# Optimization experiments

Hardware: AMD Instinct MI355X
Metric: run time of the kernel (lower is better)

Reference implementation:

```python
import jax, jax.numpy as jnp
import numpy as np

N_CODES = 1024
CODE_DIM = 256

def setup_inputs() -> dict:
    key = jax.random.key(0)
    k1, k2 = jax.random.split(key)
    z_e = jax.random.normal(k1, (16, 1024, CODE_DIM), dtype=jnp.float32)
    codebook = jax.random.normal(k2, (N_CODES, CODE_DIM), dtype=jnp.float32)
    return {"z_e": z_e, "codebook": codebook}

def reference(z_e, codebook):
    # ||z - c||^2 = ||z||^2 - 2 z.c + ||c||^2 ; ||z||^2 is constant over codes,
    # so argmin only needs -2 z.c + ||c||^2. Avoids the [B,N,n_codes,D] broadcast.
    dots = jnp.einsum('bnd,kd->bnk', z_e, codebook)          # [B, N, n_codes]
    c_sq = jnp.sum(codebook * codebook, axis=-1)             # [n_codes]
    scores = c_sq[None, None, :] - 2.0 * dots
    indices = jnp.argmin(scores, axis=-1)                    # [B, N] int
    z_q = codebook[indices]                                  # gather [B, N, D]
    # straight-through estimator
    z_q = z_e + jax.lax.stop_gradient(z_q - z_e)
    return (z_q, indices)
```

## Files before the change

### kernel.cpp

```cpp
#include <hip/hip_runtime.h>


#define M_ROWS 16384
#define DDIM   256
#define NCODES 1024

typedef _Float16 half8 __attribute__((ext_vector_type(8)));
typedef float    f32x4 __attribute__((ext_vector_type(4)));

__device__ __forceinline__ unsigned umin2(unsigned a, unsigned b) { return a < b ? a : b; }
__device__ __forceinline__ unsigned umax2(unsigned a, unsigned b) { return a > b ? a : b; }
__device__ __forceinline__ void top2_merge(unsigned& k0, unsigned& k1,
                                           unsigned o0, unsigned o1) {
    const unsigned t = umax2(k0, o0);
    k0 = umin2(k0, o0);
    k1 = umin2(t, umin2(k1, o1));
}

#define DPP_SELF(k, ctrl) \
    ((unsigned)__builtin_amdgcn_update_dpp((int)(k), (int)(k), (ctrl), 0xF, 0xF, false))
#define DPP_Z(v, ctrl) \
    __builtin_amdgcn_update_dpp(0, (v), (ctrl), 0xF, 0xF, true)

__device__ __forceinline__ float dpp_radd(float x) {
    float s = x;
    s += __int_as_float(DPP_Z(__float_as_int(s), 0x111));
    s += __int_as_float(DPP_Z(__float_as_int(s), 0x112));
    s += __int_as_float(DPP_Z(__float_as_int(s), 0x114));
    s += __int_as_float(DPP_Z(__float_as_int(s), 0x118));
    s += __int_as_float(DPP_Z(__float_as_int(s), 0x142));
    s += __int_as_float(DPP_Z(__float_as_int(s), 0x143));
    return s;
}

__global__ __launch_bounds__(256) void vq_prep_cb(const float* __restrict__ cb,
                                                  _Float16* __restrict__ chp,
                                                  float* __restrict__ csq) {
    if (blockIdx.x < 128) {
        const int gid = blockIdx.x * 256 + threadIdx.x;
        const int l   = gid & 63;
        const int g   = gid >> 6;
        const int kt  = g & 7;
        const int rt  = g >> 3;
        const int row = rt * 16 + (l & 15);
        const int k0  = kt * 32 + (l >> 4) * 8;
        const float4 v0 = *reinterpret_cast<const float4*>(cb + (size_t)row * DDIM + k0);
        const float4 v1 = *reinterpret_cast<const float4*>(cb + (size_t)row * DDIM + k0 + 4);
        half8 h;
        h[0] = (_Float16)v0.x; h[1] = (_Float16)v0.y; h[2] = (_Float16)v0.z; h[3] = (_Float16)v0.w;
        h[4] = (_Float16)v1.x; h[5] = (_Float16)v1.y; h[6] = (_Float16)v1.z; h[7] = (_Float16)v1.w;
        *reinterpret_cast<half8*>(chp + (size_t)gid * 8) = h;
    } else {
        const int code = (blockIdx.x - 128) * 4 + (threadIdx.x >> 6);
        const int lane = threadIdx.x & 63;
        const float4 v = *reinterpret_cast<const float4*>(cb + (size_t)code * DDIM + lane * 4);
        float s = v.x * v.x + v.y * v.y + v.z * v.z + v.w * v.w;
        s = dpp_radd(s);
        if (lane == 63) csq[code] = s;
    }
}

__global__ __launch_bounds__(1024) void vq_fused(const float* __restrict__ z,
                                                 const _Float16* __restrict__ Bp,
                                                 const float* __restrict__ cb,
                                                 const float* __restrict__ csq,
                                                 float* __restrict__ zq,
                                                 float* __restrict__ outIdx) {
    __shared__ __align__(16) _Float16 Ah[64 * 256];
    __shared__ uint2 red[16][64];

    const int tid  = threadIdx.x;
    const int lane = tid & 63;
    const int wv   = tid >> 6;
    const int rowBase = blockIdx.x * 64;

#pragma unroll
    for (int i = 0; i < 2; ++i) {
        const int slot = i * 1024 + tid;
        const int l  = slot & 63;
        const int g  = slot >> 6;
        const int m  = g >> 3;
        const int kt = g & 7;
        const int row = rowBase + m * 16 + (l & 15);
        const int k0  = kt * 32 + (l >> 4) * 8;
        const float4 v0 = *reinterpret_cast<const float4*>(z + (size_t)row * DDIM + k0);
        const float4 v1 = *reinterpret_cast<const float4*>(z + (size_t)row * DDIM + k0 + 4);
        half8 h;
        h[0] = (_Float16)(-v0.x); h[1] = (_Float16)(-v0.y);
        h[2] = (_Float16)(-v0.z); h[3] = (_Float16)(-v0.w);
        h[4] = (_Float16)(-v1.x); h[5] = (_Float16)(-v1.y);
        h[6] = (_Float16)(-v1.z); h[7] = (_Float16)(-v1.w);
        *reinterpret_cast<half8*>(&Ah[g * 512 + l * 8]) = h;
    }
    __syncthreads();

    const half8* __restrict__ B = reinterpret_cast<const half8*>(Bp);
    const int cx = lane & 15;
    const int q  = lane >> 4;
    const int colTile = wv;
    const int colBase = colTile * 64;

    unsigned idxv[4];
    float    bias[4];
#pragma unroll
    for (int n = 0; n < 4; ++n) {
        idxv[n] = (unsigned)(colBase + n * 16 + cx);
        bias[n] = 0.5f * csq[idxv[n]];
    }

    f32x4 acc[4][4];
#pragma unroll
    for (int m = 0; m < 4; ++m)
#pragma unroll
        for (int n = 0; n < 4; ++n)
            acc[m][n] = (f32x4){bias[n], bias[n], bias[n], bias[n]};

#pragma unroll
    for (int kt = 0; kt < 8; ++kt) {
        half8 a[4], b[4];
#pragma unroll
        for (int m = 0; m < 4; ++m)
            a[m] = *reinterpret_cast<const half8*>(&Ah[(m * 8 + kt) * 512 + lane * 8]);
#pragma unroll
        for (int n = 0; n < 4; ++n)
            b[n] = B[(size_t)(((colTile * 4 + n) * 8 + kt) * 64 + lane)];
#pragma unroll
        for (int m = 0; m < 4; ++m)
#pragma unroll
            for (int n = 0; n < 4; ++n)
                acc[m][n] = __builtin_amdgcn_mfma_f32_16x16x32_f16(a[m], b[n], acc[m][n], 0, 0, 0);
    }

#pragma unroll
    for (int m = 0; m < 4; ++m)
#pragma unroll
        for (int r = 0; r < 4; ++r) {
            const unsigned ka = (__float_as_uint(acc[m][0][r]) & 0xFFFFFC00u) | idxv[0];
            const unsigned kb = (__float_as_uint(acc[m][1][r]) & 0xFFFFFC00u) | idxv[1];
            const unsigned kc = (__float_as_uint(acc[m][2][r]) & 0xFFFFFC00u) | idxv[2];
            const unsigned kd = (__float_as_uint(acc[m][3][r]) & 0xFFFFFC00u) | idxv[3];
            const unsigned m1 = umin2(ka, kb), M1 = umax2(ka, kb);
            const unsigned m2 = umin2(kc, kd), M2 = umax2(kc, kd);
            unsigned k0 = umin2(m1, m2);
            unsigned k1 = umin2(umax2(m1, m2), umin2(M1, M2));
            top2_merge(k0, k1, DPP_SELF(k0, 0x111), DPP_SELF(k1, 0x111));
            top2_merge(k0, k1, DPP_SELF(k0, 0x112), DPP_SELF(k1, 0x112));
            top2_merge(k0, k1, DPP_SELF(k0, 0x114), DPP_SELF(k1, 0x114));
            top2_merge(k0, k1, DPP_SELF(k0, 0x118), DPP_SELF(k1, 0x118));
            if (cx == 15) red[colTile][m * 16 + q * 4 + r] = make_uint2(k0, k1);
        }
    __syncthreads();

#pragma unroll 1
    for (int i = 0; i < 4; ++i) {
        const int rl  = wv * 4 + i;
        const int row = rowBase + rl;

        unsigned kk[8];
#pragma unroll
        for (int g4 = 0; g4 < 4; ++g4) {
            const uint2 p0 = red[g4 * 4 + 0][rl], p1 = red[g4 * 4 + 1][rl];
            const uint2 p2 = red[g4 * 4 + 2][rl], p3 = red[g4 * 4 + 3][rl];
            unsigned a0 = p0.x, a1 = p0.y;
            top2_merge(a0, a1, p1.x, p1.y);
            unsigned b0 = p2.x, b1 = p2.y;
            top2_merge(b0, b1, p3.x, p3.y);
            top2_merge(a0, a1, b0, b1);
            kk[2 * g4] = a0; kk[2 * g4 + 1] = a1;
        }

        unsigned m0 = kk[0], m1 = kk[1];
        top2_merge(m0, m1, kk[2], kk[3]);
        top2_merge(m0, m1, kk[4], kk[5]);
        top2_merge(m0, m1, kk[6], kk[7]);
        const float s0 = __uint_as_float(m0 & 0xFFFFFC00u);
        const float s1 = __uint_as_float(m1 & 0xFFFFFC00u);

        if (s1 - s0 > 0.08f) {
            const int bI = (int)(m0 & 1023u);
            if (lane == 0) outIdx[row] = (float)bI;
            const float4 q4 = *reinterpret_cast<const float4*>(cb + (size_t)bI * DDIM + lane * 4);
            *reinterpret_cast<float4*>(zq + (size_t)row * DDIM + lane * 4) = q4;
            continue;
        }

        const float4 zv = *reinterpret_cast<const float4*>(z + (size_t)row * DDIM + lane * 4);

        const int idx0 = (int)(kk[0] & 1023u), idx1 = (int)(kk[1] & 1023u);
        const int idx2 = (int)(kk[2] & 1023u), idx3 = (int)(kk[3] & 1023u);
        const int idx4 = (int)(kk[4] & 1023u), idx5 = (int)(kk[5] & 1023u);
        const int idx6 = (int)(kk[6] & 1023u), idx7 = (int)(kk[7] & 1023u);
        const float4 cv0 = *reinterpret_cast<const float4*>(cb + (size_t)idx0 * DDIM + lane * 4);
        const float4 cv1 = *reinterpret_cast<const float4*>(cb + (size_t)idx1 * DDIM + lane * 4);
        const float4 cv2 = *reinterpret_cast<const float4*>(cb + (size_t)idx2 * DDIM + lane * 4);
        const float4 cv3 = *reinterpret_cast<const float4*>(cb + (size_t)idx3 * DDIM + lane * 4);
        const float4 cv4 = *reinterpret_cast<const float4*>(cb + (size_t)idx4 * DDIM + lane * 4);
        const float4 cv5 = *reinterpret_cast<const float4*>(cb + (size_t)idx5 * DDIM + lane * 4);
        const float4 cv6 = *reinterpret_cast<const float4*>(cb + (size_t)idx6 * DDIM + lane * 4);
        const float4 cv7 = *reinterpret_cast<const float4*>(cb + (size_t)idx7 * DDIM + lane * 4);

#define DOT4(cv) fmaf(zv.x, (cv).x, fmaf(zv.y, (cv).y, fmaf(zv.z, (cv).z, zv.w * (cv).w)))
        float p0 = DOT4(cv0), p1 = DOT4(cv1), p2 = DOT4(cv2), p3 = DOT4(cv3);
        float p4 = DOT4(cv4), p5 = DOT4(cv5), p6 = DOT4(cv6), p7 = DOT4(cv7);
#undef DOT4

        p0 = dpp_radd(p0); p1 = dpp_radd(p1); p2 = dpp_radd(p2); p3 = dpp_radd(p3);
        p4 = dpp_radd(p4); p5 = dpp_radd(p5); p6 = dpp_radd(p6); p7 = dpp_radd(p7);

        float bestS = fmaf(-2.0f, p0, csq[idx0]);
        int   bestI = idx0, bestC = 0;
#define CHECK(c, pc, ic)                                                     \
        {                                                                    \
            const float s = fmaf(-2.0f, (pc), csq[ic]);                      \
            const bool t = (s < bestS) || (s == bestS && (ic) < bestI);      \
            bestS = t ? s : bestS; bestI = t ? (ic) : bestI; bestC = t ? (c) : bestC; \
        }
        CHECK(1, p1, idx1) CHECK(2, p2, idx2) CHECK(3, p3, idx3)
        CHECK(4, p4, idx4) CHECK(5, p5, idx5) CHECK(6, p6, idx6) CHECK(7, p7, idx7)
#undef CHECK

        const int bI = __builtin_amdgcn_readlane(bestI, 63);
        const int bC = __builtin_amdgcn_readlane(bestC, 63);

        if (lane == 0) outIdx[row] = (float)bI;

        float4 q4 = cv0;
        if (bC == 1) q4 = cv1;
        if (bC == 2) q4 = cv2;
        if (bC == 3) q4 = cv3;
        if (bC == 4) q4 = cv4;
        if (bC == 5) q4 = cv5;
        if (bC == 6) q4 = cv6;
        if (bC == 7) q4 = cv7;
        *reinterpret_cast<float4*>(zq + (size_t)row * DDIM + lane * 4) = q4;
    }
}

extern "C" void kernel_launch(void* const* d_in, const int* in_sizes, int n_in,
                              void* d_out, int out_size, void* d_ws, size_t ws_size,
                              hipStream_t stream) {
    const float* z  = (const float*)d_in[0];
    const float* cb = (const float*)d_in[1];
    float* out    = (float*)d_out;
    float* zq     = out;
    float* outIdx = out + (size_t)M_ROWS * DDIM;

    char* ws = (char*)d_ws;
    _Float16* chp = (_Float16*)ws;
    float* csq    = (float*)(ws + 512 * 1024);

    vq_prep_cb<<<384, 256, 0, stream>>>(cb, chp, csq);
    vq_fused<<<M_ROWS / 64, 1024, 0, stream>>>(z, chp, cb, csq, zq, outIdx);
}
```

Measured before the change: 30.30 us.

## Split A staging into two K-halves to overlap second load with first-half MFMAs

The z tile is now loaded into shared memory in two halves along K. The first half is staged and synchronised, then the second half's global loads and fp16 conversion are issued before the first-half MFMA loop, and a barrier separates the two compute halves. The goal is to hide part of the global load latency of z behind matrix-core work rather than waiting for the whole tile up front. The cost is an extra block-wide barrier, and the added register pressure may limit how much the loads actually overlap.

After: 31.22 us. +3.0%, slower.

```diff
diff --git a/kernel.cpp b/kernel.cpp
--- a/kernel.cpp
+++ b/kernel.cpp
@@ -74,25 +74,41 @@
     const int wv   = tid >> 6;
     const int rowBase = blockIdx.x * 64;
 
-#pragma unroll
-    for (int i = 0; i < 2; ++i) {
-        const int slot = i * 1024 + tid;
-        const int l  = slot & 63;
-        const int g  = slot >> 6;
-        const int m  = g >> 3;
-        const int kt = g & 7;
-        const int row = rowBase + m * 16 + (l & 15);
-        const int k0  = kt * 32 + (l >> 4) * 8;
-        const float4 v0 = *reinterpret_cast<const float4*>(z + (size_t)row * DDIM + k0);
-        const float4 v1 = *reinterpret_cast<const float4*>(z + (size_t)row * DDIM + k0 + 4);
+    const int sl  = tid & 63;
+    const int gi  = tid >> 6;
+    const int sm  = gi >> 2;
+    const int skb = gi & 3;
+    const int srow = rowBase + sm * 16 + (sl & 15);
+    const int scol = (sl >> 4) * 8;
+
+    {
+        const int kt = skb;
+        const int g  = sm * 8 + kt;
+        const int k0 = kt * 32 + scol;
+        const float4 v0 = *reinterpret_cast<const float4*>(z + (size_t)srow * DDIM + k0);
+        const float4 v1 = *reinterpret_cast<const float4*>(z + (size_t)srow * DDIM + k0 + 4);
         half8 h;
         h[0] = (_Float16)(-v0.x); h[1] = (_Float16)(-v0.y);
         h[2] = (_Float16)(-v0.z); h[3] = (_Float16)(-v0.w);
         h[4] = (_Float16)(-v1.x); h[5] = (_Float16)(-v1.y);
         h[6] = (_Float16)(-v1.z); h[7] = (_Float16)(-v1.w);
-        *reinterpret_cast<half8*>(&Ah[g * 512 + l * 8]) = h;
+        *reinterpret_cast<half8*>(&Ah[g * 512 + sl * 8]) = h;
     }
     __syncthreads();
+
+    {
+        const int kt = 4 + skb;
+        const int g  = sm * 8 + kt;
+        const int k0 = kt * 32 + scol;
+        const float4 v0 = *reinterpret_cast<const float4*>(z + (size_t)srow * DDIM + k0);
+        const float4 v1 = *reinterpret_cast<const float4*>(z + (size_t)srow * DDIM + k0 + 4);
+        half8 h;
+        h[0] = (_Float16)(-v0.x); h[1] = (_Float16)(-v0.y);
+        h[2] = (_Float16)(-v0.z); h[3] = (_Float16)(-v0.w);
+        h[4] = (_Float16)(-v1.x); h[5] = (_Float16)(-v1.y);
+        h[6] = (_Float16)(-v1.z); h[7] = (_Float16)(-v1.w);
+        *reinterpret_cast<half8*>(&Ah[g * 512 + sl * 8]) = h;
+    }
 
     const half8* __restrict__ B = reinterpret_cast<const half8*>(Bp);
     const int cx = lane & 15;
@@ -116,7 +132,24 @@
             acc[m][n] = (f32x4){bias[n], bias[n], bias[n], bias[n]};
 
 #pragma unroll
-    for (int kt = 0; kt < 8; ++kt) {
+    for (int kt = 0; kt < 4; ++kt) {
+        half8 a[4], b[4];
+#pragma unroll
+        for (int m = 0; m < 4; ++m)
+            a[m] = *reinterpret_cast<const half8*>(&Ah[(m * 8 + kt) * 512 + lane * 8]);
+#pragma unroll
+        for (int n = 0; n < 4; ++n)
+            b[n] = B[(size_t)(((colTile * 4 + n) * 8 + kt) * 64 + lane)];
+#pragma unroll
+        for (int m = 0; m < 4; ++m)
+#pragma unroll
+            for (int n = 0; n < 4; ++n)
+                acc[m][n] = __builtin_amdgcn_mfma_f32_16x16x32_f16(a[m], b[n], acc[m][n], 0, 0, 0);
+    }
+    __syncthreads();
+
+#pragma unroll
+    for (int kt = 4; kt < 8; ++kt) {
         half8 a[4], b[4];
 #pragma unroll
         for (int m = 0; m < 4; ++m)
```
